# Performance work log

Measured on AMD Instinct MI355X. Metric: run time of the kernel, lower is better.

## Reference

```python
import jax, jax.numpy as jnp
import numpy as np

N_VARS = 28
HID = 64
BATCH = 32768
BN_EPS = 1e-5


def _lin_init(key, fan_in, shape):
    bound = 1.0 / np.sqrt(fan_in)
    return jax.random.uniform(key, shape, minval=-bound, maxval=bound, dtype=jnp.float32)


def setup_inputs() -> dict:
    key = jax.random.key(0)
    ks = jax.random.split(key, 8)
    n, h = N_VARS, HID
    X = jax.random.normal(ks[0], (BATCH, n), dtype=jnp.float32)
    W_logits = jax.random.uniform(ks[1], (n, n), minval=-0.01, maxval=0.01, dtype=jnp.float32)
    # per-mechanism (grouped) weights, stacked on leading mechanism axis n
    W1 = _lin_init(ks[2], n, (n, h, n)); b1 = _lin_init(ks[3], n, (n, h))
    W2 = _lin_init(ks[4], h, (n, h, h)); b2 = _lin_init(ks[5], h, (n, h))
    W3 = _lin_init(ks[6], h, (n, 1, h)); b3 = _lin_init(ks[7], h, (n, 1))
    gamma1 = jnp.ones((n, h)); beta1 = jnp.zeros((n, h))
    gamma2 = jnp.ones((n, h)); beta2 = jnp.zeros((n, h))
    return {"X": X, "W_logits": W_logits,
            "W1": W1, "b1": b1, "gamma1": gamma1, "beta1": beta1,
            "W2": W2, "b2": b2, "gamma2": gamma2, "beta2": beta2,
            "W3": W3, "b3": b3}


def _bn(x, gamma, beta):
    # x: [n, B, h]; batch stats over B (training-mode BatchNorm1d, biased var)
    m = x.mean(axis=1, keepdims=True)
    v = ((x - m) ** 2).mean(axis=1, keepdims=True)
    return gamma[:, None, :] * (x - m) * jax.lax.rsqrt(v + BN_EPS) + beta[:, None, :]


def reference(X, W_logits, W1, b1, gamma1, beta1, W2, b2, gamma2, beta2, W3, b3):
    n = W_logits.shape[0]
    # adjacency: sigmoid with zeroed diagonal
    W = jax.nn.sigmoid(W_logits) * (1.0 - jnp.eye(n, dtype=W_logits.dtype))
    # fuse the parent mask into the first layer's weights: one grouped GEMM
    # instead of n_vars separate masked matmuls
    W1_eff = W1 * W[:, None, :]                               # [n, h, n]
    h1 = jnp.einsum('bd,nhd->nbh', X, W1_eff) + b1[:, None, :]  # [n, B, h]
    a1 = jax.nn.gelu(_bn(h1, gamma1, beta1), approximate=False)
    h2 = jnp.einsum('nbh,ngh->nbg', a1, W2) + b2[:, None, :]
    a2 = jax.nn.gelu(_bn(h2, gamma2, beta2), approximate=False)
    out = jnp.einsum('nbh,noh->nbo', a2, W3) + b3[:, None, :]   # [n, B, 1]
    X_hat = out[:, :, 0].T                                     # [B, n]
    return (X_hat, W)
```

## Files before the change

### kernel.cpp

```cpp
#include <hip/hip_runtime.h>
#include <hip/hip_bf16.h>
#include <math.h>

typedef float  f4 __attribute__((ext_vector_type(4)));
typedef short  s8 __attribute__((ext_vector_type(8)));
typedef short  s4 __attribute__((ext_vector_type(4)));

#define NV 28
#define NB 32768
#define BN_EPS 1e-5f
#define NSLOT 434

#define SUM2_OFF   0
#define SSQ2_OFF   1792
#define BIAS1_OFF  3584
#define REDU_OFF   5376
#define PART_OFF   5824
#define BF_BASE_F  116992
#define W2B_OFF_S  57344
#define XBF_OFF_S  172032
#define H2_BYTE_OFF 2909184ull
#define H2_BYTES    117440512ull

__device__ __forceinline__ float gelu_f(float x) {
    float x2 = x * x;
    float z  = x * __builtin_fmaf(x2, -0.10294324f, -2.3022082f);
    float t  = __builtin_amdgcn_exp2f(z);
    return x * __builtin_amdgcn_rcpf(1.0f + t);
}
__device__ __forceinline__ unsigned short f2bf(float x) {
    unsigned u = __builtin_bit_cast(unsigned, x);
    return (unsigned short)((u + 0x7fffu + ((u >> 16) & 1u)) >> 16);
}
__device__ __forceinline__ float bf2f(short s) {
    return __builtin_bit_cast(float, ((int)(unsigned short)s) << 16);
}
__device__ __forceinline__ float row16_sum(float v) {
    int x;
    x = __builtin_amdgcn_update_dpp(0, __builtin_bit_cast(int, v), 0xB1, 0xF, 0xF, true);
    v += __builtin_bit_cast(float, x);
    x = __builtin_amdgcn_update_dpp(0, __builtin_bit_cast(int, v), 0x4E, 0xF, 0xF, true);
    v += __builtin_bit_cast(float, x);
    x = __builtin_amdgcn_update_dpp(0, __builtin_bit_cast(int, v), 0x124, 0xF, 0xF, true);
    v += __builtin_bit_cast(float, x);
    x = __builtin_amdgcn_update_dpp(0, __builtin_bit_cast(int, v), 0x128, 0xF, 0xF, true);
    v += __builtin_bit_cast(float, x);
    return v;
}
__device__ __forceinline__ float quad4_sum(float v) {
    int x;
    x = __builtin_amdgcn_update_dpp(0, __builtin_bit_cast(int, v), 0xB1, 0xF, 0xF, true);
    v += __builtin_bit_cast(float, x);
    x = __builtin_amdgcn_update_dpp(0, __builtin_bit_cast(int, v), 0x4E, 0xF, 0xF, true);
    v += __builtin_bit_cast(float, x);
    return v;
}

__global__ __launch_bounds__(256) void k_xstats(const float* __restrict__ X,
                                                float* __restrict__ ws) {
    __shared__ float sx[128 * 28];
    const int tid = threadIdx.x;
    const int rowbase = blockIdx.x * 128;
    {
        const f4* src = (const f4*)(X + (size_t)rowbase * 28);
        f4* dst = (f4*)sx;
        for (int i = tid; i < 128 * 28 / 4; i += 256) dst[i] = src[i];
    }
    __syncthreads();
    int* xb = (int*)((short*)(ws + BF_BASE_F) + XBF_OFF_S);
    for (int j = tid; j < 128 * 16; j += 256) {
        int row = j >> 4, cc = j & 15;
        float lo = (2 * cc     < 28) ? sx[row * 28 + 2 * cc]     : 0.0f;
        float hi = (2 * cc + 1 < 28) ? sx[row * 28 + 2 * cc + 1] : 0.0f;
        xb[(size_t)(rowbase + row) * 16 + cc] = (int)f2bf(lo) | ((int)f2bf(hi) << 16);
    }
    for (int s = tid; s < NSLOT; s += 256) {
        float a = 0.0f;
        if (s < 28) {
            for (int r = 0; r < 128; ++r) a += sx[r * 28 + s];
        } else {
            int p = s - 28, d = 0, rem = 28;
            while (p >= rem) { p -= rem; ++d; --rem; }
            int e = d + p;
            for (int r = 0; r < 128; ++r)
                a = __builtin_fmaf(sx[r * 28 + d], sx[r * 28 + e], a);
        }
        ws[PART_OFF + blockIdx.x * NSLOT + s] = a;
    }
}

__global__ __launch_bounds__(256) void k_reduce(float* __restrict__ ws) {
    int s = blockIdx.x * 256 + threadIdx.x;
    if (s < NSLOT) {
        float a = 0.0f;
#pragma unroll 16
        for (int p = 0; p < 256; ++p) a += ws[PART_OFF + p * NSLOT + s];
        ws[REDU_OFF + s] = a;
    }
}

__global__ __launch_bounds__(256) void k_fold1(const float* __restrict__ Wlog,
                                               const float* __restrict__ W1,
                                               const float* __restrict__ g1,
                                               const float* __restrict__ be1,
                                               const float* __restrict__ W2,
                                               float* __restrict__ ws,
                                               float* __restrict__ out_w) {
    __shared__ float mu[28], wrow[28];
    __shared__ float C[784];
    __shared__ float w1e_s[64 * 28];
    const int n = blockIdx.x, t = threadIdx.x;

    if (t < 28) {
        mu[t] = ws[REDU_OFF + t] * (1.0f / 32768.0f);
        float w = 1.0f / (1.0f + expf(-Wlog[n * 28 + t]));
        if (t == n) w = 0.0f;
        wrow[t] = w;
        out_w[n * 28 + t] = w;
    }
    if (t < 64) {
        ws[SUM2_OFF + n * 64 + t] = 0.0f;
        ws[SSQ2_OFF + n * 64 + t] = 0.0f;
    }
    __syncthreads();
    for (int i = t; i < 784; i += 256) {
        int d = i / 28, e = i % 28;
        int lo = d < e ? d : e, hi = d < e ? e : d;
        int idx = 28 + lo * 28 - (lo * (lo - 1)) / 2 + (hi - lo);
        C[i] = ws[REDU_OFF + idx] * (1.0f / 32768.0f) - mu[d] * mu[e];
    }
    for (int i = t; i < 1792; i += 256)
        w1e_s[i] = W1[(size_t)n * 1792 + i] * wrow[i % 28];
    __syncthreads();

    const int h = t >> 2, j = t & 3;
    const float* we = &w1e_s[h * 28];
    float var_p = 0.0f, dot_p = 0.0f;
#pragma unroll
    for (int k = 0; k < 7; ++k) {
        int d = 7 * j + k;
        float inner = 0.0f;
#pragma unroll
        for (int e = 0; e < 28; ++e) inner = __builtin_fmaf(C[d * 28 + e], we[e], inner);
        float wd = we[d];
        var_p = __builtin_fmaf(inner, wd, var_p);
        dot_p = __builtin_fmaf(wd, mu[d], dot_p);
    }
    float var  = quad4_sum(var_p);
    float dotm = quad4_sum(dot_p);
    float scale = g1[n * 64 + h] * rsqrtf(fmaxf(var, 0.0f) + BN_EPS);
    if (j == 0)
        ws[BIAS1_OFF + n * 64 + h] = be1[n * 64 + h] - dotm * scale;

    short* bfbase = (short*)(ws + BF_BASE_F);
    {
        short* w1f = bfbase + (size_t)(n * 64 + h) * 32;
        s8 pk;
#pragma unroll
        for (int k = 0; k < 8; ++k) {
            int d = 8 * j + k;
            pk[k] = (short)f2bf(d < 28 ? we[d] * scale : 0.0f);
        }
        *(s8*)&w1f[8 * j] = pk;
    }
    {
        const float* w2src = W2 + (size_t)n * 4096 + t * 16;
        short* w2d = bfbase + W2B_OFF_S + (size_t)n * 4096 + t * 16;
        s8 a, b;
#pragma unroll
        for (int k = 0; k < 8; ++k) a[k] = (short)f2bf(w2src[k]);
#pragma unroll
        for (int k = 0; k < 8; ++k) b[k] = (short)f2bf(w2src[8 + k]);
        *(s8*)&w2d[0] = a;
        *(s8*)&w2d[8] = b;
    }
}

template <bool STORE>
__global__ __launch_bounds__(256, 4) void k_pass1(float* __restrict__ ws,
                                                  short* __restrict__ h2buf) {
    __shared__ __align__(16) short sW1[64 * 40];
    __shared__ __align__(16) short sW2[64 * 72];
    __shared__ __align__(16) short sA1[8 * 16 * 72];
    __shared__ float sP1[4][64], sP2[4][64];

    const int n = blockIdx.x >> 7;
    const int blk = blockIdx.x & 127;
    const int tid = threadIdx.x;
    const int wave = tid >> 6;
    const int lane = tid & 63;
    const int m = lane & 15;
    const int q = lane >> 4;

    const short* bfbase = (const short*)(ws + BF_BASE_F);
    const short* w1g = bfbase + (size_t)n * 64 * 32;
    const short* w2g = bfbase + W2B_OFF_S + (size_t)n * 64 * 64;
    const short* xbf = bfbase + XBF_OFF_S;
    {
        int r = tid >> 2, c = tid & 3;
        *(s8*)&sW1[r * 40 + c * 8] = *(const s8*)&w1g[r * 32 + c * 8];
#pragma unroll
        for (int k = 0; k < 2; ++k) {
            int i2 = tid + k * 256;
            int r2 = i2 >> 3, c2 = i2 & 7;
            *(s8*)&sW2[r2 * 72 + c2 * 8] = *(const s8*)&w2g[r2 * 64 + c2 * 8];
        }
    }
    __syncthreads();

    const float* bias1 = ws + BIAS1_OFF + n * 64;
    short* myA1a = &sA1[(wave * 2 + 0) * 16 * 72];
    short* myA1b = &sA1[(wave * 2 + 1) * 16 * 72];
    float s1[16], s2v[16];
#pragma unroll
    for (int i = 0; i < 16; ++i) { s1[i] = 0.0f; s2v[i] = 0.0f; }

#pragma unroll
    for (int it = 0; it < 2; ++it) {
        const int row0 = blk * 256 + it * 128 + wave * 32;
        s8 xfa = *(const s8*)&xbf[(size_t)(row0 + m) * 32 + 8 * q];
        s8 xfb = *(const s8*)&xbf[(size_t)(row0 + 16 + m) * 32 + 8 * q];

        f4 acc1a[4], acc1b[4];
#pragma unroll
        for (int t = 0; t < 4; ++t) {
            s8 wf = *(const s8*)&sW1[(16 * t + m) * 40 + q * 8];
            acc1a[t] = __builtin_amdgcn_mfma_f32_16x16x32_bf16(wf, xfa, (f4){0.f, 0.f, 0.f, 0.f}, 0, 0, 0);
            acc1b[t] = __builtin_amdgcn_mfma_f32_16x16x32_bf16(wf, xfb, (f4){0.f, 0.f, 0.f, 0.f}, 0, 0, 0);
        }
#pragma unroll
        for (int t = 0; t < 4; ++t) {
            f4 bv = *(const f4*)&bias1[16 * t + 4 * q];
            s4 pa, pb;
#pragma unroll
            for (int r = 0; r < 4; ++r) {
                pa[r] = (short)f2bf(gelu_f(acc1a[t][r] + bv[r]));
                pb[r] = (short)f2bf(gelu_f(acc1b[t][r] + bv[r]));
            }
            *(s4*)&myA1a[m * 72 + 16 * t + 4 * q] = pa;
            *(s4*)&myA1b[m * 72 + 16 * t + 4 * q] = pb;
        }
        s8 af0a = *(const s8*)&myA1a[m * 72 + 8 * q];
        s8 af1a = *(const s8*)&myA1a[m * 72 + 32 + 8 * q];
        s8 af0b = *(const s8*)&myA1b[m * 72 + 8 * q];
        s8 af1b = *(const s8*)&myA1b[m * 72 + 32 + 8 * q];
        short* hpA = STORE ? (h2buf + ((size_t)n * NB + row0 + m) * 64) : nullptr;
        short* hpB = STORE ? (h2buf + ((size_t)n * NB + row0 + 16 + m) * 64) : nullptr;
#pragma unroll
        for (int u = 0; u < 4; ++u) {
            s8 w0 = *(const s8*)&sW2[(16 * u + m) * 72 + 8 * q];
            s8 w1 = *(const s8*)&sW2[(16 * u + m) * 72 + 32 + 8 * q];
            f4 aa = (f4){0.f, 0.f, 0.f, 0.f};
            f4 ab = (f4){0.f, 0.f, 0.f, 0.f};
            aa = __builtin_amdgcn_mfma_f32_16x16x32_bf16(w0, af0a, aa, 0, 0, 0);
            ab = __builtin_amdgcn_mfma_f32_16x16x32_bf16(w0, af0b, ab, 0, 0, 0);
            aa = __builtin_amdgcn_mfma_f32_16x16x32_bf16(w1, af1a, aa, 0, 0, 0);
            ab = __builtin_amdgcn_mfma_f32_16x16x32_bf16(w1, af1b, ab, 0, 0, 0);
            if (STORE) {
                s4 ha, hb;
#pragma unroll
                for (int r = 0; r < 4; ++r) { ha[r] = (short)f2bf(aa[r]); hb[r] = (short)f2bf(ab[r]); }
                *(s4*)&hpA[16 * u + 4 * q] = ha;
                *(s4*)&hpB[16 * u + 4 * q] = hb;
            }
#pragma unroll
            for (int r = 0; r < 4; ++r) {
                s1[u * 4 + r]  += aa[r] + ab[r];
                s2v[u * 4 + r] = __builtin_fmaf(aa[r], aa[r], s2v[u * 4 + r]);
                s2v[u * 4 + r] = __builtin_fmaf(ab[r], ab[r], s2v[u * 4 + r]);
            }
        }
    }
#pragma unroll
    for (int u = 0; u < 4; ++u) {
#pragma unroll
        for (int r = 0; r < 4; ++r) {
            float t1 = row16_sum(s1[u * 4 + r]);
            float t2 = row16_sum(s2v[u * 4 + r]);
            if (m == 0) {
                sP1[wave][16 * u + 4 * q + r] = t1;
                sP2[wave][16 * u + 4 * q + r] = t2;
            }
        }
    }
    __syncthreads();
    if (tid < 64) {
        float a = sP1[0][tid] + sP1[1][tid] + sP1[2][tid] + sP1[3][tid];
        float b = sP2[0][tid] + sP2[1][tid] + sP2[2][tid] + sP2[3][tid];
        atomicAdd(&ws[SUM2_OFF + n * 64 + tid], a);
        atomicAdd(&ws[SSQ2_OFF + n * 64 + tid], b);
    }
}

__global__ __launch_bounds__(256) void k_pass2s(const float* __restrict__ g2,
                                                const float* __restrict__ be2,
                                                const float* __restrict__ W3,
                                                const float* __restrict__ b3,
                                                const float* __restrict__ ws,
                                                const short* __restrict__ h2buf,
                                                float* __restrict__ out) {
    __shared__ float sSc[64], sSh[64], sW3v[64];
    const int n = blockIdx.x >> 7;
    const int row = ((blockIdx.x & 127) << 8) + threadIdx.x;
    if (threadIdx.x < 64) {
        int g = threadIdx.x;
        float mean = ws[SUM2_OFF + n * 64 + g] * (1.0f / 32768.0f);
        float var  = ws[SSQ2_OFF + n * 64 + g] * (1.0f / 32768.0f) - mean * mean;
        float sc = g2[n * 64 + g] * rsqrtf(fmaxf(var, 0.0f) + BN_EPS);
        sSc[g]  = sc;
        sSh[g]  = be2[n * 64 + g] - mean * sc;
        sW3v[g] = W3[n * 64 + g];
    }
    __syncthreads();
    const short* hp = h2buf + ((size_t)n * NB + row) * 64;
    float p = 0.0f;
#pragma unroll
    for (int c = 0; c < 8; ++c) {
        s8 hv = *(const s8*)&hp[c * 8];
#pragma unroll
        for (int k = 0; k < 8; ++k) {
            int g = c * 8 + k;
            float v = bf2f(hv[k]);
            p = __builtin_fmaf(gelu_f(__builtin_fmaf(v, sSc[g], sSh[g])), sW3v[g], p);
        }
    }
    out[(size_t)row * 28 + n] = p + b3[n];
}

__global__ __launch_bounds__(256, 4) void k_pass2r(const float* __restrict__ g2,
                                                   const float* __restrict__ be2,
                                                   const float* __restrict__ W3,
                                                   const float* __restrict__ b3,
                                                   float* __restrict__ ws,
                                                   float* __restrict__ out) {
    __shared__ __align__(16) short sW1[64 * 40];
    __shared__ __align__(16) short sW2[64 * 72];
    __shared__ __align__(16) short sA1[8 * 16 * 72];
    __shared__ float sSc[64], sSh[64], sW3v[64];

    const int n = blockIdx.x >> 7;
    const int blk = blockIdx.x & 127;
    const int tid = threadIdx.x;
    const int wave = tid >> 6;
    const int lane = tid & 63;
    const int m = lane & 15;
    const int q = lane >> 4;

    const short* bfbase = (const short*)(ws + BF_BASE_F);
    const short* w1g = bfbase + (size_t)n * 64 * 32;
    const short* w2g = bfbase + W2B_OFF_S + (size_t)n * 64 * 64;
    const short* xbf = bfbase + XBF_OFF_S;
    {
        int r = tid >> 2, c = tid & 3;
        *(s8*)&sW1[r * 40 + c * 8] = *(const s8*)&w1g[r * 32 + c * 8];
#pragma unroll
        for (int k = 0; k < 2; ++k) {
            int i2 = tid + k * 256;
            int r2 = i2 >> 3, c2 = i2 & 7;
            *(s8*)&sW2[r2 * 72 + c2 * 8] = *(const s8*)&w2g[r2 * 64 + c2 * 8];
        }
        if (tid < 64) {
            float mean = ws[SUM2_OFF + n * 64 + tid] * (1.0f / 32768.0f);
            float var  = ws[SSQ2_OFF + n * 64 + tid] * (1.0f / 32768.0f) - mean * mean;
            float sc = g2[n * 64 + tid] * rsqrtf(fmaxf(var, 0.0f) + BN_EPS);
            sSc[tid]  = sc;
            sSh[tid]  = be2[n * 64 + tid] - mean * sc;
            sW3v[tid] = W3[n * 64 + tid];
        }
    }
    __syncthreads();

    const float* bias1 = ws + BIAS1_OFF + n * 64;
    const float b3n = b3[n];
    short* myA1a = &sA1[(wave * 2 + 0) * 16 * 72];
    short* myA1b = &sA1[(wave * 2 + 1) * 16 * 72];

#pragma unroll
    for (int it = 0; it < 2; ++it) {
        const int row0 = blk * 256 + it * 128 + wave * 32;
        s8 xfa = *(const s8*)&xbf[(size_t)(row0 + m) * 32 + 8 * q];
        s8 xfb = *(const s8*)&xbf[(size_t)(row0 + 16 + m) * 32 + 8 * q];

        f4 acc1a[4], acc1b[4];
#pragma unroll
        for (int t = 0; t < 4; ++t) {
            s8 wf = *(const s8*)&sW1[(16 * t + m) * 40 + q * 8];
            acc1a[t] = __builtin_amdgcn_mfma_f32_16x16x32_bf16(wf, xfa, (f4){0.f, 0.f, 0.f, 0.f}, 0, 0, 0);
            acc1b[t] = __builtin_amdgcn_mfma_f32_16x16x32_bf16(wf, xfb, (f4){0.f, 0.f, 0.f, 0.f}, 0, 0, 0);
        }
#pragma unroll
        for (int t = 0; t < 4; ++t) {
            f4 bv = *(const f4*)&bias1[16 * t + 4 * q];
            s4 pa, pb;
#pragma unroll
            for (int r = 0; r < 4; ++r) {
                pa[r] = (short)f2bf(gelu_f(acc1a[t][r] + bv[r]));
                pb[r] = (short)f2bf(gelu_f(acc1b[t][r] + bv[r]));
            }
            *(s4*)&myA1a[m * 72 + 16 * t + 4 * q] = pa;
            *(s4*)&myA1b[m * 72 + 16 * t + 4 * q] = pb;
        }
        s8 af0a = *(const s8*)&myA1a[m * 72 + 8 * q];
        s8 af1a = *(const s8*)&myA1a[m * 72 + 32 + 8 * q];
        s8 af0b = *(const s8*)&myA1b[m * 72 + 8 * q];
        s8 af1b = *(const s8*)&myA1b[m * 72 + 32 + 8 * q];
        float pa = 0.0f, pb = 0.0f;
#pragma unroll
        for (int u = 0; u < 4; ++u) {
            s8 w0 = *(const s8*)&sW2[(16 * u + m) * 72 + 8 * q];
            s8 w1 = *(const s8*)&sW2[(16 * u + m) * 72 + 32 + 8 * q];
            f4 aa = (f4){0.f, 0.f, 0.f, 0.f};
            f4 ab = (f4){0.f, 0.f, 0.f, 0.f};
            aa = __builtin_amdgcn_mfma_f32_16x16x32_bf16(w0, af0a, aa, 0, 0, 0);
            ab = __builtin_amdgcn_mfma_f32_16x16x32_bf16(w0, af0b, ab, 0, 0, 0);
            aa = __builtin_amdgcn_mfma_f32_16x16x32_bf16(w1, af1a, aa, 0, 0, 0);
            ab = __builtin_amdgcn_mfma_f32_16x16x32_bf16(w1, af1b, ab, 0, 0, 0);
            f4 scv = *(const f4*)&sSc[16 * u + 4 * q];
            f4 shv = *(const f4*)&sSh[16 * u + 4 * q];
            f4 w3v = *(const f4*)&sW3v[16 * u + 4 * q];
#pragma unroll
            for (int r = 0; r < 4; ++r) {
                float va = __builtin_fmaf(aa[r], scv[r], shv[r]);
                float vb = __builtin_fmaf(ab[r], scv[r], shv[r]);
                pa = __builtin_fmaf(gelu_f(va), w3v[r], pa);
                pb = __builtin_fmaf(gelu_f(vb), w3v[r], pb);
            }
        }
        pa += __shfl_xor(pa, 16);  pa += __shfl_xor(pa, 32);
        pb += __shfl_xor(pb, 16);  pb += __shfl_xor(pb, 32);
        if (q == 0) {
            out[(size_t)(row0 + m) * 28 + n]      = pa + b3n;
            out[(size_t)(row0 + 16 + m) * 28 + n] = pb + b3n;
        }
    }
}

extern "C" void kernel_launch(void* const* d_in, const int* in_sizes, int n_in,
                              void* d_out, int out_size, void* d_ws, size_t ws_size,
                              hipStream_t stream) {
    const float* X   = (const float*)d_in[0];
    const float* Wl  = (const float*)d_in[1];
    const float* W1  = (const float*)d_in[2];
    const float* g1  = (const float*)d_in[4];
    const float* be1 = (const float*)d_in[5];
    const float* W2  = (const float*)d_in[6];
    const float* g2  = (const float*)d_in[8];
    const float* be2 = (const float*)d_in[9];
    const float* W3  = (const float*)d_in[10];
    const float* b3  = (const float*)d_in[11];
    float* out = (float*)d_out;
    float* ws  = (float*)d_ws;
    short* h2buf = (short*)((char*)d_ws + H2_BYTE_OFF);
    const bool store_h2 = ws_size >= H2_BYTE_OFF + H2_BYTES;

    k_xstats<<<dim3(256), dim3(256), 0, stream>>>(X, ws);
    k_reduce<<<dim3(2), dim3(256), 0, stream>>>(ws);
    k_fold1<<<dim3(28), dim3(256), 0, stream>>>(Wl, W1, g1, be1, W2, ws, out + 917504);
    if (store_h2) {
        k_pass1<true><<<dim3(28 * 128), dim3(256), 0, stream>>>(ws, h2buf);
        k_pass2s<<<dim3(28 * 128), dim3(256), 0, stream>>>(g2, be2, W3, b3, ws, h2buf, out);
    } else {
        k_pass1<false><<<dim3(28 * 128), dim3(256), 0, stream>>>(ws, nullptr);
        k_pass2r<<<dim3(28 * 128), dim3(256), 0, stream>>>(g2, be2, W3, b3, ws, out);
    }
}
```

Baseline: 187.4 us.

## Restructure pass2 so each thread writes contiguous output rows, and raise pass1 occupancy

Pass2 is rewritten so each wave handles 7 mechanisms for 64 rows, and each thread writes 7 contiguous outputs per row instead of one strided float. The per-mechanism BN2 scale and shift move into a separate small k_fold2 kernel that stores them in the workspace. Pass1 shrinks its shared A1 buffer by reusing one tile for both halves and keeps the bias in registers. It also drops the block-level reduction in favour of per-wave atomics, and raises launch bounds to 6 blocks per CU. The trade-offs are an extra kernel launch, more atomic traffic, and register pressure under the tighter occupancy target.

```diff
diff --git a/kernel.cpp b/kernel.cpp
--- a/kernel.cpp
+++ b/kernel.cpp
@@ -15,11 +15,13 @@
 #define SSQ2_OFF   1792
 #define BIAS1_OFF  3584
 #define REDU_OFF   5376
-#define PART_OFF   5824
-#define BF_BASE_F  116992
+#define SC2_OFF    5824
+#define SH2_OFF    7616
+#define PART_OFF   9472
+#define BF_BASE_F  120640
 #define W2B_OFF_S  57344
 #define XBF_OFF_S  172032
-#define H2_BYTE_OFF 2909184ull
+#define H2_BYTE_OFF 2924544ull
 #define H2_BYTES    117440512ull
 
 __device__ __forceinline__ float gelu_f(float x) {
@@ -177,12 +179,11 @@
 }
 
 template <bool STORE>
-__global__ __launch_bounds__(256, 4) void k_pass1(float* __restrict__ ws,
+__global__ __launch_bounds__(256, 6) void k_pass1(float* __restrict__ ws,
                                                   short* __restrict__ h2buf) {
     __shared__ __align__(16) short sW1[64 * 40];
     __shared__ __align__(16) short sW2[64 * 72];
-    __shared__ __align__(16) short sA1[8 * 16 * 72];
-    __shared__ float sP1[4][64], sP2[4][64];
+    __shared__ __align__(16) short sA1[4 * 16 * 72];
 
     const int n = blockIdx.x >> 7;
     const int blk = blockIdx.x & 127;
@@ -209,8 +210,11 @@
     __syncthreads();
 
     const float* bias1 = ws + BIAS1_OFF + n * 64;
-    short* myA1a = &sA1[(wave * 2 + 0) * 16 * 72];
-    short* myA1b = &sA1[(wave * 2 + 1) * 16 * 72];
+    f4 biasv[4];
+#pragma unroll
+    for (int t = 0; t < 4; ++t) biasv[t] = *(const f4*)&bias1[16 * t + 4 * q];
+
+    short* myA1 = &sA1[wave * 16 * 72];
     float s1[16], s2v[16];
 #pragma unroll
     for (int i = 0; i < 16; ++i) { s1[i] = 0.0f; s2v[i] = 0.0f; }
@@ -228,22 +232,24 @@
             acc1a[t] = __builtin_amdgcn_mfma_f32_16x16x32_bf16(wf, xfa, (f4){0.f, 0.f, 0.f, 0.f}, 0, 0, 0);
             acc1b[t] = __builtin_amdgcn_mfma_f32_16x16x32_bf16(wf, xfb, (f4){0.f, 0.f, 0.f, 0.f}, 0, 0, 0);
         }
+        s4 pka[4], pkb[4];
 #pragma unroll
         for (int t = 0; t < 4; ++t) {
-            f4 bv = *(const f4*)&bias1[16 * t + 4 * q];
-            s4 pa, pb;
 #pragma unroll
             for (int r = 0; r < 4; ++r) {
-                pa[r] = (short)f2bf(gelu_f(acc1a[t][r] + bv[r]));
-                pb[r] = (short)f2bf(gelu_f(acc1b[t][r] + bv[r]));
-            }
-            *(s4*)&myA1a[m * 72 + 16 * t + 4 * q] = pa;
-            *(s4*)&myA1b[m * 72 + 16 * t + 4 * q] = pb;
-        }
-        s8 af0a = *(const s8*)&myA1a[m * 72 + 8 * q];
-        s8 af1a = *(const s8*)&myA1a[m * 72 + 32 + 8 * q];
-        s8 af0b = *(const s8*)&myA1b[m * 72 + 8 * q];
-        s8 af1b = *(const s8*)&myA1b[m * 72 + 32 + 8 * q];
+                pka[t][r] = (short)f2bf(gelu_f(acc1a[t][r] + biasv[t][r]));
+                pkb[t][r] = (short)f2bf(gelu_f(acc1b[t][r] + biasv[t][r]));
+            }
+        }
+#pragma unroll
+        for (int t = 0; t < 4; ++t) *(s4*)&myA1[m * 72 + 16 * t + 4 * q] = pka[t];
+        s8 af0a = *(const s8*)&myA1[m * 72 + 8 * q];
+        s8 af1a = *(const s8*)&myA1[m * 72 + 32 + 8 * q];
+#pragma unroll
+        for (int t = 0; t < 4; ++t) *(s4*)&myA1[m * 72 + 16 * t + 4 * q] = pkb[t];
+        s8 af0b = *(const s8*)&myA1[m * 72 + 8 * q];
+        s8 af1b = *(const s8*)&myA1[m * 72 + 32 + 8 * q];
+
         short* hpA = STORE ? (h2buf + ((size_t)n * NB + row0 + m) * 64) : nullptr;
         short* hpB = STORE ? (h2buf + ((size_t)n * NB + row0 + 16 + m) * 64) : nullptr;
 #pragma unroll
@@ -278,53 +284,57 @@
             float t1 = row16_sum(s1[u * 4 + r]);
             float t2 = row16_sum(s2v[u * 4 + r]);
             if (m == 0) {
-                sP1[wave][16 * u + 4 * q + r] = t1;
-                sP2[wave][16 * u + 4 * q + r] = t2;
-            }
-        }
-    }
-    __syncthreads();
-    if (tid < 64) {
-        float a = sP1[0][tid] + sP1[1][tid] + sP1[2][tid] + sP1[3][tid];
-        float b = sP2[0][tid] + sP2[1][tid] + sP2[2][tid] + sP2[3][tid];
-        atomicAdd(&ws[SUM2_OFF + n * 64 + tid], a);
-        atomicAdd(&ws[SSQ2_OFF + n * 64 + tid], b);
-    }
-}
-
-__global__ __launch_bounds__(256) void k_pass2s(const float* __restrict__ g2,
-                                                const float* __restrict__ be2,
-                                                const float* __restrict__ W3,
+                atomicAdd(&ws[SUM2_OFF + n * 64 + 16 * u + 4 * q + r], t1);
+                atomicAdd(&ws[SSQ2_OFF + n * 64 + 16 * u + 4 * q + r], t2);
+            }
+        }
+    }
+}
+
+__global__ void k_fold2(const float* __restrict__ g2, const float* __restrict__ be2,
+                        float* __restrict__ ws) {
+    int i = blockIdx.x * 256 + threadIdx.x;
+    if (i < 1792) {
+        float mean = ws[SUM2_OFF + i] * (1.0f / 32768.0f);
+        float var  = ws[SSQ2_OFF + i] * (1.0f / 32768.0f) - mean * mean;
+        float sc = g2[i] * rsqrtf(fmaxf(var, 0.0f) + BN_EPS);
+        ws[SC2_OFF + i] = sc;
+        ws[SH2_OFF + i] = be2[i] - mean * sc;
+    }
+}
+
+__global__ __launch_bounds__(256) void k_pass2t(const float* __restrict__ W3,
                                                 const float* __restrict__ b3,
                                                 const float* __restrict__ ws,
                                                 const short* __restrict__ h2buf,
                                                 float* __restrict__ out) {
-    __shared__ float sSc[64], sSh[64], sW3v[64];
-    const int n = blockIdx.x >> 7;
-    const int row = ((blockIdx.x & 127) << 8) + threadIdx.x;
-    if (threadIdx.x < 64) {
-        int g = threadIdx.x;
-        float mean = ws[SUM2_OFF + n * 64 + g] * (1.0f / 32768.0f);
-        float var  = ws[SSQ2_OFF + n * 64 + g] * (1.0f / 32768.0f) - mean * mean;
-        float sc = g2[n * 64 + g] * rsqrtf(fmaxf(var, 0.0f) + BN_EPS);
-        sSc[g]  = sc;
-        sSh[g]  = be2[n * 64 + g] - mean * sc;
-        sW3v[g] = W3[n * 64 + g];
-    }
-    __syncthreads();
-    const short* hp = h2buf + ((size_t)n * NB + row) * 64;
-    float p = 0.0f;
-#pragma unroll
-    for (int c = 0; c < 8; ++c) {
-        s8 hv = *(const s8*)&hp[c * 8];
-#pragma unroll
-        for (int k = 0; k < 8; ++k) {
-            int g = c * 8 + k;
-            float v = bf2f(hv[k]);
-            p = __builtin_fmaf(gelu_f(__builtin_fmaf(v, sSc[g], sSh[g])), sW3v[g], p);
-        }
-    }
-    out[(size_t)row * 28 + n] = p + b3[n];
+    const int lane = threadIdx.x & 63;
+    const int wv = __builtin_amdgcn_readfirstlane(threadIdx.x >> 6);
+    const int row = blockIdx.x * 64 + lane;
+    const float* sc2 = ws + SC2_OFF;
+    const float* sh2 = ws + SH2_OFF;
+    float res[7];
+#pragma unroll
+    for (int k = 0; k < 7; ++k) {
+        const int n = wv * 7 + k;
+        const short* hp = h2buf + ((size_t)n * NB + row) * 64;
+        float p0 = 0.0f, p1 = 0.0f;
+#pragma unroll
+        for (int c = 0; c < 8; ++c) {
+            s8 hv = *(const s8*)&hp[c * 8];
+#pragma unroll
+            for (int j = 0; j < 8; ++j) {
+                const int g = n * 64 + c * 8 + j;
+                float v = __builtin_fmaf(bf2f(hv[j]), sc2[g], sh2[g]);
+                if (j & 1) p1 = __builtin_fmaf(gelu_f(v), W3[g], p1);
+                else       p0 = __builtin_fmaf(gelu_f(v), W3[g], p0);
+            }
+        }
+        res[k] = p0 + p1 + b3[n];
+    }
+    float* op = out + (size_t)row * 28 + wv * 7;
+#pragma unroll
+    for (int k = 0; k < 7; ++k) op[k] = res[k];
 }
 
 __global__ __launch_bounds__(256, 4) void k_pass2r(const float* __restrict__ g2,
@@ -458,7 +468,8 @@
     k_fold1<<<dim3(28), dim3(256), 0, stream>>>(Wl, W1, g1, be1, W2, ws, out + 917504);
     if (store_h2) {
         k_pass1<true><<<dim3(28 * 128), dim3(256), 0, stream>>>(ws, h2buf);
-        k_pass2s<<<dim3(28 * 128), dim3(256), 0, stream>>>(g2, be2, W3, b3, ws, h2buf, out);
+        k_fold2<<<dim3(7), dim3(256), 0, stream>>>(g2, be2, ws);
+        k_pass2t<<<dim3(512), dim3(256), 0, stream>>>(W3, b3, ws, h2buf, out);
     } else {
         k_pass1<false><<<dim3(28 * 128), dim3(256), 0, stream>>>(ws, nullptr);
         k_pass2r<<<dim3(28 * 128), dim3(256), 0, stream>>>(g2, be2, W3, b3, ws, out);
```

New measurement: 352.5 us. 1.88x slower.
